# Performance work log

Measured on AMD Instinct MI355X. Metric: run time of the kernel, lower is better.

The kernel has to match this reference:

```python
import jax, jax.numpy as jnp
import numpy as np

EMB = 1024
HID = 2048
N_EXPERTS = 8
CAPACITY_FACTOR = 1.25
Z_LOSS_COEFF = 0.001


def setup_inputs() -> dict:
    key = jax.random.key(0)
    ks = jax.random.split(key, 8)
    B, T = 8, 4096
    x = jax.random.normal(ks[0], (B, T, EMB), dtype=jnp.float32)
    s_r = 1.0 / np.sqrt(EMB)
    s_h = 1.0 / np.sqrt(HID)
    wr = jax.random.uniform(ks[1], (EMB, N_EXPERTS), jnp.float32, -s_r, s_r)
    br = jax.random.uniform(ks[2], (N_EXPERTS,), jnp.float32, -s_r, s_r)
    w1 = jax.random.uniform(ks[3], (N_EXPERTS, EMB, HID), jnp.float32, -s_r, s_r)
    b1 = jax.random.uniform(ks[4], (N_EXPERTS, HID), jnp.float32, -s_r, s_r)
    w2 = jax.random.uniform(ks[5], (N_EXPERTS, HID, EMB), jnp.float32, -s_h, s_h)
    b2 = jax.random.uniform(ks[6], (N_EXPERTS, EMB), jnp.float32, -s_h, s_h)
    return {"x": x, "wr": wr, "br": br, "w1": w1, "b1": b1, "w2": w2, "b2": b2, "k": 2}


def reference(x, wr, br, w1, b1, w2, b2, k):
    B, T, D = x.shape
    E = wr.shape[1]
    N = B * T
    cap = int(CAPACITY_FACTOR * N / E)

    # Router
    logits = jnp.einsum("btd,de->bte", x, wr) + br
    probs = jax.nn.softmax(logits, axis=-1)
    z_loss = Z_LOSS_COEFF * jnp.mean(logits * logits)
    _, topk_idx = jax.lax.top_k(probs, k)  # [B,T,k]

    xf = x.reshape(N, D)
    idx = topk_idx.reshape(N, k)

    # mask[e, n]: token n routed to expert e (any of its top-k slots)
    mask = (idx[None, :, :] == jnp.arange(E, dtype=idx.dtype)[:, None, None]).any(-1)
    pos = jnp.cumsum(mask.astype(jnp.int32), axis=1) - 1  # rank within expert (flattened order)
    keep = mask & (pos < cap)  # capacity truncation: keep first `cap` tokens per expert

    # buf[e, c] = flat index of c-th kept token for expert e, or N (pad)
    cols = jnp.where(keep, pos, cap)  # dropped/unrouted tokens go to dump column
    rows = jnp.broadcast_to(jnp.arange(E)[:, None], (E, N))
    toks_id = jnp.broadcast_to(jnp.arange(N, dtype=jnp.int32)[None, :], (E, N))
    buf = jnp.full((E, cap + 1), N, dtype=jnp.int32).at[rows, cols].set(toks_id)[:, :cap]

    # Dispatch (gather), per-expert dense FFN, combine (scatter-add)
    x_pad = jnp.concatenate([xf, jnp.zeros((1, D), x.dtype)], axis=0)
    toks = x_pad[buf]  # [E, cap, D]
    h = jax.nn.gelu(jnp.einsum("ecd,edh->ech", toks, w1) + b1[:, None, :], approximate=False)
    out = jnp.einsum("ech,ehd->ecd", h, w2) + b2[:, None, :]  # [E, cap, D]
    out_flat = jnp.zeros((N + 1, D), x.dtype).at[buf.reshape(-1)].add(out.reshape(-1, D))[:N]
    output = out_flat.reshape(B, T, D)

    expert_usage = keep.sum(axis=1).astype(jnp.float32)  # [E]
    load = expert_usage / (expert_usage.sum() + 1e-6)
    balance_loss = E * jnp.sum(load * load)
    return output, balance_loss + z_loss, expert_usage
```

## Files before the change

kernel.cpp:

```cpp
#include <hip/hip_runtime.h>
#include <cstdint>

#define NTOK   32768
#define EMB_D  1024
#define HID_H  2048
#define NEXP   8
#define CAP    5120
#define MROWS  (NEXP * CAP)
#define NCHUNK 32

typedef __bf16 bf16_t;
typedef bf16_t bf16x8 __attribute__((ext_vector_type(8)));
typedef float  f32x4  __attribute__((ext_vector_type(4)));

typedef __attribute__((address_space(3))) void       lds_void_t;
typedef const __attribute__((address_space(1))) void g_void_t;

__device__ __forceinline__ void gload_lds16(const void* g, void* l) {
    __builtin_amdgcn_global_load_lds((g_void_t*)(uintptr_t)g,
                                     (lds_void_t*)(uint32_t)(uintptr_t)l, 16, 0, 0);
}

__global__ void router_kernel(const float* __restrict__ x, const float* __restrict__ wr,
                              const float* __restrict__ br, int2* __restrict__ top2,
                              float* __restrict__ zsum) {
    __shared__ float s_wr[NEXP * EMB_D];
    __shared__ float s_z[4];
    const int tid = threadIdx.x;
    for (int i = tid; i < NEXP * EMB_D; i += 256) {
        int d = i >> 3, e = i & 7;
        s_wr[e * EMB_D + d] = wr[i];
    }
    __syncthreads();
    const int wid = tid >> 6, lane = tid & 63;
    const int t = blockIdx.x * 4 + wid;
    const float* xr = x + (size_t)t * EMB_D;

    float acc[NEXP];
#pragma unroll
    for (int e = 0; e < NEXP; e++) acc[e] = 0.f;
#pragma unroll
    for (int it = 0; it < EMB_D / 64; ++it) {
        float xv = xr[lane + 64 * it];
#pragma unroll
        for (int e = 0; e < NEXP; e++) acc[e] += xv * s_wr[e * EMB_D + lane + 64 * it];
    }
#pragma unroll
    for (int e = 0; e < NEXP; e++) {
        float v = acc[e];
#pragma unroll
        for (int off = 32; off > 0; off >>= 1) v += __shfl_xor(v, off);
        acc[e] = v;
    }
    if (lane == 0) {
        float lg[NEXP]; float zs = 0.f;
#pragma unroll
        for (int e = 0; e < NEXP; e++) { lg[e] = acc[e] + br[e]; zs += lg[e] * lg[e]; }
        s_z[wid] = zs;
        float mx = lg[0];
        for (int e = 1; e < NEXP; e++) mx = fmaxf(mx, lg[e]);
        float p[NEXP]; float se = 0.f;
        for (int e = 0; e < NEXP; e++) { p[e] = expf(lg[e] - mx); se += p[e]; }
        for (int e = 0; e < NEXP; e++) p[e] = p[e] / se;
        int i0 = 0; float b0 = p[0];
        for (int e = 1; e < NEXP; e++) if (p[e] > b0) { b0 = p[e]; i0 = e; }
        int i1 = -1; float b1v = -1.f;
        for (int e = 0; e < NEXP; e++) if (e != i0 && p[e] > b1v) { b1v = p[e]; i1 = e; }
        top2[t] = make_int2(i0, i1);
    }
    __syncthreads();
    if (tid == 0) unsafeAtomicAdd(zsum, s_z[0] + s_z[1] + s_z[2] + s_z[3]);
}

__global__ void count_kernel(const int2* __restrict__ top2, int* __restrict__ counts) {
    const int chunk = blockIdx.x;
    const int tid = threadIdx.x;
    const int wid = tid >> 6, lane = tid & 63;
    __shared__ int wcnt[NEXP][16];
    const int2 tp = top2[chunk * 1024 + tid];
#pragma unroll
    for (int e = 0; e < NEXP; e++) {
        const bool m = (tp.x == e) || (tp.y == e);
        unsigned long long bal = __ballot(m);
        if (lane == 0) wcnt[e][wid] = __popcll(bal);
    }
    __syncthreads();
    if (tid < NEXP) {
        int s = 0;
        for (int w = 0; w < 16; w++) s += wcnt[tid][w];
        counts[chunk * NEXP + tid] = s;
    }
}

__global__ void prefix_kernel(const int* __restrict__ counts, int* __restrict__ base,
                              int* __restrict__ usage) {
    const int e = threadIdx.x;
    if (e < NEXP) {
        int run = 0;
        for (int c = 0; c < NCHUNK; c++) {
            base[c * NEXP + e] = run;
            run += counts[c * NEXP + e];
        }
        usage[e] = run < CAP ? run : CAP;
    }
}

__global__ void place_kernel(const int2* __restrict__ top2, const int* __restrict__ base,
                             int* __restrict__ buf, int* __restrict__ inv) {
    const int chunk = blockIdx.x;
    const int tid = threadIdx.x;
    const int wid = tid >> 6, lane = tid & 63;
    const int t = chunk * 1024 + tid;
    __shared__ int wpre[NEXP][16];
    const int2 tp = top2[t];
    int lpre[NEXP]; bool mm[NEXP];
#pragma unroll
    for (int e = 0; e < NEXP; e++) {
        mm[e] = (tp.x == e) || (tp.y == e);
        unsigned long long bal = __ballot(mm[e]);
        lpre[e] = __popcll(bal & ((1ull << lane) - 1ull));
        if (lane == 0) wpre[e][wid] = __popcll(bal);
    }
    __syncthreads();
    if (tid < NEXP) {
        int a = 0;
        for (int w = 0; w < 16; w++) { int v = wpre[tid][w]; wpre[tid][w] = a; a += v; }
    }
    __syncthreads();
#pragma unroll
    for (int e = 0; e < NEXP; e++) {
        if (mm[e]) {
            const int pos = base[chunk * NEXP + e] + wpre[e][wid] + lpre[e];
            const int slot = (tp.x == e) ? 0 : 1;
            if (pos < CAP) {
                const int row = e * CAP + pos;
                buf[row] = t;
                inv[t * 2 + slot] = row;
            } else {
                inv[t * 2 + slot] = -1;
            }
        }
    }
}

__global__ void pad_kernel(const int* __restrict__ usage, int* __restrict__ buf) {
    const int e = blockIdx.x;
    const int u = usage[e];
    for (int p = u + threadIdx.x; p < CAP; p += blockDim.x) buf[e * CAP + p] = NTOK;
}

__global__ void gather_kernel(const float* __restrict__ x, const int* __restrict__ buf,
                              bf16_t* __restrict__ Xg) {
    const int row = blockIdx.x;
    const int t = buf[row];
    const int tid = threadIdx.x;
    bf16x8 v;
    if (t >= 0 && t < NTOK) {
        const float* xr = x + (size_t)t * EMB_D + tid * 8;
        const float4 a = *(const float4*)(xr);
        const float4 b = *(const float4*)(xr + 4);
        v[0] = (bf16_t)a.x; v[1] = (bf16_t)a.y; v[2] = (bf16_t)a.z; v[3] = (bf16_t)a.w;
        v[4] = (bf16_t)b.x; v[5] = (bf16_t)b.y; v[6] = (bf16_t)b.z; v[7] = (bf16_t)b.w;
    } else {
#pragma unroll
        for (int i = 0; i < 8; i++) v[i] = (bf16_t)0.f;
    }
    *(bf16x8*)(Xg + (size_t)row * EMB_D + tid * 8) = v;
}

__global__ void transpose_conv_kernel(const float* __restrict__ in, bf16_t* __restrict__ out,
                                      int R, int C) {
    __shared__ bf16_t tile[64][72];
    const int e = blockIdx.z;
    const int c0 = blockIdx.x * 64, r0 = blockIdx.y * 64;
    const float*  ip = in  + (size_t)e * R * C;
    bf16_t*       op = out + (size_t)e * R * C;
    const int tid = threadIdx.x;
    const int tr = tid >> 4;
    const int tc = (tid & 15) * 4;
#pragma unroll
    for (int rr = 0; rr < 64; rr += 16) {
        const float4 v = *(const float4*)(ip + (size_t)(r0 + tr + rr) * C + (c0 + tc));
        tile[tr + rr][tc + 0] = (bf16_t)v.x;
        tile[tr + rr][tc + 1] = (bf16_t)v.y;
        tile[tr + rr][tc + 2] = (bf16_t)v.z;
        tile[tr + rr][tc + 3] = (bf16_t)v.w;
    }
    __syncthreads();
    const int oc = tid >> 2;
    const int og = (tid & 3) * 16;
    bf16x8 v0, v1;
#pragma unroll
    for (int i = 0; i < 8; i++) v0[i] = tile[og + i][oc];
#pragma unroll
    for (int i = 0; i < 8; i++) v1[i] = tile[og + 8 + i][oc];
    *(bf16x8*)(op + (size_t)(c0 + oc) * R + r0 + og)     = v0;
    *(bf16x8*)(op + (size_t)(c0 + oc) * R + r0 + og + 8) = v1;
}

#define BUF_BYTES 65536
#define LDS_TOTAL 131072

__device__ __forceinline__ const bf16x8* fragp(const char* base, int row, int ks, int quad) {
    return (const bf16x8*)(base + row * 128 + ((((ks << 2) + quad) ^ (row & 7)) << 4));
}

__device__ __forceinline__ void stage_ht(const bf16_t* __restrict__ Ap,
                                         const bf16_t* __restrict__ Bp,
                                         int K, int NT, char* lds0, int idx, int tid) {
    if (idx >= 4 * NT) return;
    const int t = idx >> 2, part = idx & 3;
    char* dst = lds0 + (t & 1) * BUF_BYTES + ((part < 2) ? 32768 : 0)
              + (part & 1) * 16384 + tid * 16;
    const int row0 = tid >> 3;
    const int sq   = (tid & 7) ^ (row0 & 7);
    const bf16_t* src = ((part < 2) ? Bp : Ap)
                      + (size_t)((part & 1) * 128 + row0) * K + (size_t)t * 64 + sq * 8;
    gload_lds16(src, dst);
    gload_lds16(src + (size_t)64 * K, dst + 8192);
}

template <int NT>
__device__ __forceinline__ void mainloop256(const bf16_t* __restrict__ Ap,
                                            const bf16_t* __restrict__ Bp,
                                            char* lds0, f32x4 (&acc)[8][4]) {
    const int K = NT * 64;
    const int tid = threadIdx.x;
    const int lane = tid & 63, wid = tid >> 6;
    const int wm = wid >> 2, wn = wid & 3;
    const int quad = lane >> 4, l16 = lane & 15;

#pragma unroll
    for (int idx = 0; idx < 6; ++idx) stage_ht(Ap, Bp, K, NT, lds0, idx, tid);
    asm volatile("s_waitcnt vmcnt(4)" ::: "memory");
    __builtin_amdgcn_s_barrier();

    bf16x8 a[8], bl[4], bh[4];
    for (int t = 0; t < NT; ++t) {
        const char* bufA = lds0 + (t & 1) * BUF_BYTES;
        const char* bufB = bufA + 32768;
        const int pbase = 4 * t + 6;

#pragma unroll
        for (int mf = 0; mf < 4; ++mf)
#pragma unroll
            for (int ks = 0; ks < 2; ++ks)
                a[mf * 2 + ks] = *fragp(bufA, wm * 128 + mf * 16 + l16, ks, quad);
#pragma unroll
        for (int nf = 0; nf < 2; ++nf)
#pragma unroll
            for (int ks = 0; ks < 2; ++ks)
                bl[nf * 2 + ks] = *fragp(bufB, wn * 64 + nf * 16 + l16, ks, quad);
        stage_ht(Ap, Bp, K, NT, lds0, pbase + 0, tid);
        __builtin_amdgcn_s_barrier();
        asm volatile("s_waitcnt lgkmcnt(0)" ::: "memory");
        __builtin_amdgcn_sched_barrier(0);
        __builtin_amdgcn_s_setprio(1);
#pragma unroll
        for (int mf = 0; mf < 4; ++mf)
#pragma unroll
            for (int nf = 0; nf < 2; ++nf)
#pragma unroll
                for (int ks = 0; ks < 2; ++ks)
                    acc[mf][nf] = __builtin_amdgcn_mfma_f32_16x16x32_bf16(
                        a[mf * 2 + ks], bl[nf * 2 + ks], acc[mf][nf], 0, 0, 0);
        __builtin_amdgcn_s_setprio(0);
        __builtin_amdgcn_s_barrier();

#pragma unroll
        for (int nf = 0; nf < 2; ++nf)
#pragma unroll
            for (int ks = 0; ks < 2; ++ks)
                bh[nf * 2 + ks] = *fragp(bufB, wn * 64 + (nf + 2) * 16 + l16, ks, quad);
        stage_ht(Ap, Bp, K, NT, lds0, pbase + 1, tid);
        __builtin_amdgcn_s_barrier();
        asm volatile("s_waitcnt lgkmcnt(0)" ::: "memory");
        __builtin_amdgcn_sched_barrier(0);
        __builtin_amdgcn_s_setprio(1);
#pragma unroll
        for (int mf = 0; mf < 4; ++mf)
#pragma unroll
            for (int nf = 0; nf < 2; ++nf)
#pragma unroll
                for (int ks = 0; ks < 2; ++ks)
                    acc[mf][nf + 2] = __builtin_amdgcn_mfma_f32_16x16x32_bf16(
                        a[mf * 2 + ks], bh[nf * 2 + ks], acc[mf][nf + 2], 0, 0, 0);
        __builtin_amdgcn_s_setprio(0);
        __builtin_amdgcn_s_barrier();

#pragma unroll
        for (int mf = 0; mf < 4; ++mf)
#pragma unroll
            for (int ks = 0; ks < 2; ++ks)
                a[mf * 2 + ks] = *fragp(bufA, wm * 128 + (mf + 4) * 16 + l16, ks, quad);
        stage_ht(Ap, Bp, K, NT, lds0, pbase + 2, tid);
        __builtin_amdgcn_s_barrier();
        asm volatile("s_waitcnt lgkmcnt(0)" ::: "memory");
        __builtin_amdgcn_sched_barrier(0);
        __builtin_amdgcn_s_setprio(1);
#pragma unroll
        for (int mf = 0; mf < 4; ++mf)
#pragma unroll
            for (int nf = 0; nf < 2; ++nf)
#pragma unroll
                for (int ks = 0; ks < 2; ++ks)
                    acc[mf + 4][nf + 2] = __builtin_amdgcn_mfma_f32_16x16x32_bf16(
                        a[mf * 2 + ks], bh[nf * 2 + ks], acc[mf + 4][nf + 2], 0, 0, 0);
        __builtin_amdgcn_s_setprio(0);
        __builtin_amdgcn_s_barrier();

        stage_ht(Ap, Bp, K, NT, lds0, pbase + 3, tid);
        __builtin_amdgcn_s_setprio(1);
#pragma unroll
        for (int mf = 0; mf < 4; ++mf)
#pragma unroll
            for (int nf = 0; nf < 2; ++nf)
#pragma unroll
                for (int ks = 0; ks < 2; ++ks)
                    acc[mf + 4][nf] = __builtin_amdgcn_mfma_f32_16x16x32_bf16(
                        a[mf * 2 + ks], bl[nf * 2 + ks], acc[mf + 4][nf], 0, 0, 0);
        __builtin_amdgcn_s_setprio(0);
        asm volatile("s_waitcnt vmcnt(4)" ::: "memory");
        __builtin_amdgcn_s_barrier();
    }
}

__global__ __launch_bounds__(512, 2) void gemm1_kernel(const bf16_t* __restrict__ Xg,
                                                       const bf16_t* __restrict__ w1t,
                                                       const float* __restrict__ b1,
                                                       bf16_t* __restrict__ H) {
    extern __shared__ char lds0[];
    const int bn = blockIdx.x, bm = blockIdx.y;
    const int e = bm / (CAP / 256);
    const bf16_t* Ap = Xg + (size_t)bm * 256 * EMB_D;
    const bf16_t* Bp = w1t + ((size_t)e * HID_H + bn * 256) * EMB_D;
    f32x4 acc[8][4];
    const f32x4 z4 = {0.f, 0.f, 0.f, 0.f};
#pragma unroll
    for (int i = 0; i < 8; i++)
#pragma unroll
        for (int j = 0; j < 4; j++) acc[i][j] = z4;

    mainloop256<EMB_D / 64>(Ap, Bp, lds0, acc);

    const int tid = threadIdx.x;
    const int lane = tid & 63, wid = tid >> 6;
    const int wm = wid >> 2, wn = wid & 3;
    const int quad = lane >> 4, l16 = lane & 15;
#pragma unroll
    for (int nf = 0; nf < 4; ++nf) {
        const int col = bn * 256 + wn * 64 + nf * 16 + l16;
        const float bias = b1[e * HID_H + col];
#pragma unroll
        for (int mf = 0; mf < 8; ++mf) {
            const int row = bm * 256 + wm * 128 + mf * 16 + quad * 4;
#pragma unroll
            for (int r = 0; r < 4; ++r) {
                const float v = acc[mf][nf][r] + bias;
                const float g = 0.5f * v * (1.f + erff(v * 0.7071067811865475f));
                H[(size_t)(row + r) * HID_H + col] = (bf16_t)g;
            }
        }
    }
}

__global__ __launch_bounds__(512, 2) void gemm2_kernel(const bf16_t* __restrict__ H,
                                                       const bf16_t* __restrict__ w2t,
                                                       bf16_t* __restrict__ Yg) {
    extern __shared__ char lds0[];
    const int bn = blockIdx.x, bm = blockIdx.y;
    const int e = bm / (CAP / 256);
    const bf16_t* Ap = H + (size_t)bm * 256 * HID_H;
    const bf16_t* Bp = w2t + ((size_t)e * EMB_D + bn * 256) * HID_H;
    f32x4 acc[8][4];
    const f32x4 z4 = {0.f, 0.f, 0.f, 0.f};
#pragma unroll
    for (int i = 0; i < 8; i++)
#pragma unroll
        for (int j = 0; j < 4; j++) acc[i][j] = z4;

    mainloop256<HID_H / 64>(Ap, Bp, lds0, acc);

    const int tid = threadIdx.x;
    const int lane = tid & 63, wid = tid >> 6;
    const int wm = wid >> 2, wn = wid & 3;
    const int quad = lane >> 4, l16 = lane & 15;
#pragma unroll
    for (int nf = 0; nf < 4; ++nf) {
        const int col = bn * 256 + wn * 64 + nf * 16 + l16;
#pragma unroll
        for (int mf = 0; mf < 8; ++mf) {
            const int row = bm * 256 + wm * 128 + mf * 16 + quad * 4;
#pragma unroll
            for (int r = 0; r < 4; ++r)
                Yg[(size_t)(row + r) * EMB_D + col] = (bf16_t)acc[mf][nf][r];
        }
    }
}

__global__ void combine_kernel(const bf16_t* __restrict__ Yg, const float* __restrict__ b2,
                               const int* __restrict__ inv, float* __restrict__ out) {
    const int t = blockIdx.x;
    const int tid = threadIdx.x;
    const int d = tid * 8;
    const int r0 = inv[t * 2], r1 = inv[t * 2 + 1];
    float acc[8];
#pragma unroll
    for (int i = 0; i < 8; i++) acc[i] = 0.f;
    if (r0 >= 0) {
        const int e = r0 / CAP;
        const bf16x8 v = *(const bf16x8*)(Yg + (size_t)r0 * EMB_D + d);
        const float* bp = b2 + e * EMB_D + d;
#pragma unroll
        for (int i = 0; i < 8; i++) acc[i] += (float)v[i] + bp[i];
    }
    if (r1 >= 0) {
        const int e = r1 / CAP;
        const bf16x8 v = *(const bf16x8*)(Yg + (size_t)r1 * EMB_D + d);
        const float* bp = b2 + e * EMB_D + d;
#pragma unroll
        for (int i = 0; i < 8; i++) acc[i] += (float)v[i] + bp[i];
    }
    float4 o0 = {acc[0], acc[1], acc[2], acc[3]};
    float4 o1 = {acc[4], acc[5], acc[6], acc[7]};
    *(float4*)(out + (size_t)t * EMB_D + d)     = o0;
    *(float4*)(out + (size_t)t * EMB_D + d + 4) = o1;
}

__global__ void finalize_kernel(const int* __restrict__ usage, const float* __restrict__ zsum,
                                float* __restrict__ out) {
    if (threadIdx.x == 0) {
        float u[NEXP], s = 0.f;
        for (int e = 0; e < NEXP; e++) { u[e] = (float)usage[e]; s += u[e]; }
        const float inv = 1.f / (s + 1e-6f);
        float bal = 0.f;
        for (int e = 0; e < NEXP; e++) { const float l = u[e] * inv; bal += l * l; }
        bal *= (float)NEXP;
        const float z = 0.001f * zsum[0] / (float)((size_t)NTOK * NEXP);
        out[(size_t)NTOK * EMB_D] = bal + z;
        for (int e = 0; e < NEXP; e++) out[(size_t)NTOK * EMB_D + 1 + e] = u[e];
    }
}

extern "C" void kernel_launch(void* const* d_in, const int* in_sizes, int n_in,
                              void* d_out, int out_size, void* d_ws, size_t ws_size,
                              hipStream_t stream) {
    (void)in_sizes; (void)n_in; (void)out_size;
    const float* x  = (const float*)d_in[0];
    const float* wr = (const float*)d_in[1];
    const float* br = (const float*)d_in[2];
    const float* w1 = (const float*)d_in[3];
    const float* b1 = (const float*)d_in[4];
    const float* w2 = (const float*)d_in[5];
    const float* b2 = (const float*)d_in[6];
    float* out = (float*)d_out;

    uint8_t* ws = (uint8_t*)d_ws;
    size_t off = 0;
    auto carve = [&](size_t bytes) -> void* {
        off = (off + 255) & ~(size_t)255;
        void* p = ws + off;
        off += bytes;
        return p;
    };
    float*  zsum  = (float*)carve(sizeof(float));
    int*    usage = (int*)carve(NEXP * sizeof(int));
    int*    counts = (int*)carve((size_t)NCHUNK * NEXP * sizeof(int));
    int*    base   = (int*)carve((size_t)NCHUNK * NEXP * sizeof(int));
    int2*   top2 = (int2*)carve((size_t)NTOK * sizeof(int2));
    int*    buf  = (int*)carve((size_t)MROWS * sizeof(int));
    int*    inv  = (int*)carve((size_t)NTOK * 2 * sizeof(int));
    bf16_t* Xg   = (bf16_t*)carve((size_t)MROWS * EMB_D * sizeof(bf16_t));
    bf16_t* w1t  = (bf16_t*)carve((size_t)NEXP * HID_H * EMB_D * sizeof(bf16_t));
    bf16_t* w2t  = (bf16_t*)carve((size_t)NEXP * EMB_D * HID_H * sizeof(bf16_t));
    bf16_t* H    = (bf16_t*)carve((size_t)MROWS * HID_H * sizeof(bf16_t));
    bf16_t* Yg   = Xg;
    if (off > ws_size) return;

    static bool attr_set = false;
    if (!attr_set) {
        hipFuncSetAttribute(reinterpret_cast<const void*>(&gemm1_kernel),
                            hipFuncAttributeMaxDynamicSharedMemorySize, LDS_TOTAL);
        hipFuncSetAttribute(reinterpret_cast<const void*>(&gemm2_kernel),
                            hipFuncAttributeMaxDynamicSharedMemorySize, LDS_TOTAL);
        attr_set = true;
    }

    hipMemsetAsync(zsum, 0, sizeof(float), stream);

    router_kernel<<<NTOK / 4, 256, 0, stream>>>(x, wr, br, top2, zsum);
    count_kernel<<<NCHUNK, 1024, 0, stream>>>(top2, counts);
    prefix_kernel<<<1, 64, 0, stream>>>(counts, base, usage);
    place_kernel<<<NCHUNK, 1024, 0, stream>>>(top2, base, buf, inv);
    pad_kernel<<<NEXP, 256, 0, stream>>>(usage, buf);
    gather_kernel<<<MROWS, 128, 0, stream>>>(x, buf, Xg);
    transpose_conv_kernel<<<dim3(HID_H / 64, EMB_D / 64, NEXP), 256, 0, stream>>>(w1, w1t, EMB_D, HID_H);
    transpose_conv_kernel<<<dim3(EMB_D / 64, HID_H / 64, NEXP), 256, 0, stream>>>(w2, w2t, HID_H, EMB_D);
    gemm1_kernel<<<dim3(HID_H / 256, MROWS / 256), 512, LDS_TOTAL, stream>>>(Xg, w1t, b1, H);
    gemm2_kernel<<<dim3(EMB_D / 256, MROWS / 256), 512, LDS_TOTAL, stream>>>(H, w2t, Yg);
    combine_kernel<<<NTOK, 128, 0, stream>>>(Yg, b2, inv, out);
    finalize_kernel<<<1, 64, 0, stream>>>(usage, zsum, out);
}
```

Measured before the change: 907.6 us.

## Restructure GEMM mainloop into two half-phases and stage epilogue through LDS

```diff
diff --git a/kernel.cpp b/kernel.cpp
--- a/kernel.cpp
+++ b/kernel.cpp
@@ -205,19 +205,17 @@
     return (const bf16x8*)(base + row * 128 + ((((ks << 2) + quad) ^ (row & 7)) << 4));
 }
 
-__device__ __forceinline__ void stage_ht(const bf16_t* __restrict__ Ap,
-                                         const bf16_t* __restrict__ Bp,
-                                         int K, int NT, char* lds0, int idx, int tid) {
-    if (idx >= 4 * NT) return;
-    const int t = idx >> 2, part = idx & 3;
-    char* dst = lds0 + (t & 1) * BUF_BYTES + ((part < 2) ? 32768 : 0)
-              + (part & 1) * 16384 + tid * 16;
+__device__ __forceinline__ void stage_panel(const bf16_t* __restrict__ P, int K,
+                                            char* lds0, int dstpar, int isB,
+                                            int srct, int tid) {
+    char* dst = lds0 + dstpar * BUF_BYTES + (isB ? 32768 : 0) + tid * 16;
     const int row0 = tid >> 3;
     const int sq   = (tid & 7) ^ (row0 & 7);
-    const bf16_t* src = ((part < 2) ? Bp : Ap)
-                      + (size_t)((part & 1) * 128 + row0) * K + (size_t)t * 64 + sq * 8;
+    const bf16_t* src = P + (size_t)row0 * K + (size_t)srct * 64 + sq * 8;
     gload_lds16(src, dst);
-    gload_lds16(src + (size_t)64 * K, dst + 8192);
+    gload_lds16(src + (size_t)64 * K,  dst + 8192);
+    gload_lds16(src + (size_t)128 * K, dst + 16384);
+    gload_lds16(src + (size_t)192 * K, dst + 24576);
 }
 
 template <int NT>
@@ -230,98 +228,112 @@
     const int wm = wid >> 2, wn = wid & 3;
     const int quad = lane >> 4, l16 = lane & 15;
 
-#pragma unroll
-    for (int idx = 0; idx < 6; ++idx) stage_ht(Ap, Bp, K, NT, lds0, idx, tid);
+    stage_panel(Bp, K, lds0, 0, 1, 0, tid);
+    stage_panel(Ap, K, lds0, 0, 0, 0, tid);
+    stage_panel(Bp, K, lds0, 1, 1, (NT > 1 ? 1 : 0), tid);
     asm volatile("s_waitcnt vmcnt(4)" ::: "memory");
     __builtin_amdgcn_s_barrier();
 
-    bf16x8 a[8], bl[4], bh[4];
+    bf16x8 aa[8], bb[8];
     for (int t = 0; t < NT; ++t) {
         const char* bufA = lds0 + (t & 1) * BUF_BYTES;
         const char* bufB = bufA + 32768;
-        const int pbase = 4 * t + 6;
 
 #pragma unroll
         for (int mf = 0; mf < 4; ++mf)
 #pragma unroll
             for (int ks = 0; ks < 2; ++ks)
-                a[mf * 2 + ks] = *fragp(bufA, wm * 128 + mf * 16 + l16, ks, quad);
-#pragma unroll
-        for (int nf = 0; nf < 2; ++nf)
+                aa[mf * 2 + ks] = *fragp(bufA, wm * 128 + mf * 16 + l16, ks, quad);
+#pragma unroll
+        for (int nf = 0; nf < 4; ++nf)
 #pragma unroll
             for (int ks = 0; ks < 2; ++ks)
-                bl[nf * 2 + ks] = *fragp(bufB, wn * 64 + nf * 16 + l16, ks, quad);
-        stage_ht(Ap, Bp, K, NT, lds0, pbase + 0, tid);
-        __builtin_amdgcn_s_barrier();
+                bb[nf * 2 + ks] = *fragp(bufB, wn * 64 + nf * 16 + l16, ks, quad);
+        stage_panel(Ap, K, lds0, (t + 1) & 1, 0, (t + 1 < NT ? t + 1 : 0), tid);
         asm volatile("s_waitcnt lgkmcnt(0)" ::: "memory");
         __builtin_amdgcn_sched_barrier(0);
         __builtin_amdgcn_s_setprio(1);
 #pragma unroll
         for (int mf = 0; mf < 4; ++mf)
 #pragma unroll
-            for (int nf = 0; nf < 2; ++nf)
+            for (int nf = 0; nf < 4; ++nf)
 #pragma unroll
                 for (int ks = 0; ks < 2; ++ks)
                     acc[mf][nf] = __builtin_amdgcn_mfma_f32_16x16x32_bf16(
-                        a[mf * 2 + ks], bl[nf * 2 + ks], acc[mf][nf], 0, 0, 0);
+                        aa[mf * 2 + ks], bb[nf * 2 + ks], acc[mf][nf], 0, 0, 0);
         __builtin_amdgcn_s_setprio(0);
         __builtin_amdgcn_s_barrier();
 
 #pragma unroll
-        for (int nf = 0; nf < 2; ++nf)
+        for (int mf = 0; mf < 4; ++mf)
 #pragma unroll
             for (int ks = 0; ks < 2; ++ks)
-                bh[nf * 2 + ks] = *fragp(bufB, wn * 64 + (nf + 2) * 16 + l16, ks, quad);
-        stage_ht(Ap, Bp, K, NT, lds0, pbase + 1, tid);
-        __builtin_amdgcn_s_barrier();
+                aa[mf * 2 + ks] = *fragp(bufA, wm * 128 + (mf + 4) * 16 + l16, ks, quad);
+        stage_panel(Bp, K, lds0, t & 1, 1, (t + 2 < NT ? t + 2 : t + 2 - NT), tid);
         asm volatile("s_waitcnt lgkmcnt(0)" ::: "memory");
         __builtin_amdgcn_sched_barrier(0);
         __builtin_amdgcn_s_setprio(1);
 #pragma unroll
         for (int mf = 0; mf < 4; ++mf)
 #pragma unroll
-            for (int nf = 0; nf < 2; ++nf)
-#pragma unroll
-                for (int ks = 0; ks < 2; ++ks)
-                    acc[mf][nf + 2] = __builtin_amdgcn_mfma_f32_16x16x32_bf16(
-                        a[mf * 2 + ks], bh[nf * 2 + ks], acc[mf][nf + 2], 0, 0, 0);
-        __builtin_amdgcn_s_setprio(0);
-        __builtin_amdgcn_s_barrier();
-
-#pragma unroll
-        for (int mf = 0; mf < 4; ++mf)
-#pragma unroll
-            for (int ks = 0; ks < 2; ++ks)
-                a[mf * 2 + ks] = *fragp(bufA, wm * 128 + (mf + 4) * 16 + l16, ks, quad);
-        stage_ht(Ap, Bp, K, NT, lds0, pbase + 2, tid);
-        __builtin_amdgcn_s_barrier();
-        asm volatile("s_waitcnt lgkmcnt(0)" ::: "memory");
-        __builtin_amdgcn_sched_barrier(0);
-        __builtin_amdgcn_s_setprio(1);
-#pragma unroll
-        for (int mf = 0; mf < 4; ++mf)
-#pragma unroll
-            for (int nf = 0; nf < 2; ++nf)
-#pragma unroll
-                for (int ks = 0; ks < 2; ++ks)
-                    acc[mf + 4][nf + 2] = __builtin_amdgcn_mfma_f32_16x16x32_bf16(
-                        a[mf * 2 + ks], bh[nf * 2 + ks], acc[mf + 4][nf + 2], 0, 0, 0);
-        __builtin_amdgcn_s_setprio(0);
-        __builtin_amdgcn_s_barrier();
-
-        stage_ht(Ap, Bp, K, NT, lds0, pbase + 3, tid);
-        __builtin_amdgcn_s_setprio(1);
-#pragma unroll
-        for (int mf = 0; mf < 4; ++mf)
-#pragma unroll
-            for (int nf = 0; nf < 2; ++nf)
+            for (int nf = 0; nf < 4; ++nf)
 #pragma unroll
                 for (int ks = 0; ks < 2; ++ks)
                     acc[mf + 4][nf] = __builtin_amdgcn_mfma_f32_16x16x32_bf16(
-                        a[mf * 2 + ks], bl[nf * 2 + ks], acc[mf + 4][nf], 0, 0, 0);
+                        aa[mf * 2 + ks], bb[nf * 2 + ks], acc[mf + 4][nf], 0, 0, 0);
         __builtin_amdgcn_s_setprio(0);
         asm volatile("s_waitcnt vmcnt(4)" ::: "memory");
         __builtin_amdgcn_s_barrier();
+    }
+    asm volatile("s_waitcnt vmcnt(0)" ::: "memory");
+    __builtin_amdgcn_s_barrier();
+}
+
+template <int APPLY>
+__device__ __forceinline__ void epilogue_store(const f32x4 (&acc)[8][4], char* lds0,
+                                               const float* __restrict__ bias4,
+                                               bf16_t* __restrict__ Out, int ldo,
+                                               int bm, int bn) {
+    const int tid = threadIdx.x;
+    const int lane = tid & 63, wid = tid >> 6;
+    const int wm = wid >> 2, wn = wid & 3;
+    const int quad = lane >> 4, l16 = lane & 15;
+    const int l8 = lane & 7, g8 = lane >> 3;
+    char* eb = lds0 + wid * 8192;
+    const int rslot = (l8 ^ g8) << 4;
+#pragma unroll
+    for (int h = 0; h < 2; ++h) {
+#pragma unroll
+        for (int mfh = 0; mfh < 4; ++mfh) {
+#pragma unroll
+            for (int r = 0; r < 4; ++r) {
+                const int lrow = mfh * 16 + quad * 4 + r;
+#pragma unroll
+                for (int nf = 0; nf < 4; ++nf) {
+                    float v = acc[h * 4 + mfh][nf][r];
+                    if (APPLY) {
+                        v += bias4[nf];
+                        v = 0.5f * v * (1.f + erff(v * 0.7071067811865475f));
+                    }
+                    const int lcol = nf * 16 + l16;
+                    const int byte = lrow * 128 +
+                        (((lcol >> 3) ^ (lrow & 7)) << 4) + ((lcol & 7) << 1);
+                    *(bf16_t*)(eb + byte) = (bf16_t)v;
+                }
+            }
+        }
+        asm volatile("s_waitcnt lgkmcnt(0)" ::: "memory");
+        __builtin_amdgcn_sched_barrier(0);
+#pragma unroll
+        for (int i = 0; i < 8; ++i) {
+            const int rr = i * 8 + g8;
+            const bf16x8 v = *(const bf16x8*)(eb + rr * 128 + rslot);
+            const int grow = bm * 256 + wm * 128 + h * 64 + rr;
+            const int gcol = bn * 256 + wn * 64 + l8 * 8;
+            *(bf16x8*)(Out + (size_t)grow * ldo + gcol) = v;
+        }
+        asm volatile("s_waitcnt lgkmcnt(0)" ::: "memory");
+        __builtin_amdgcn_sched_barrier(0);
     }
 }
 
@@ -343,25 +355,13 @@
 
     mainloop256<EMB_D / 64>(Ap, Bp, lds0, acc);
 
-    const int tid = threadIdx.x;
-    const int lane = tid & 63, wid = tid >> 6;
-    const int wm = wid >> 2, wn = wid & 3;
-    const int quad = lane >> 4, l16 = lane & 15;
-#pragma unroll
-    for (int nf = 0; nf < 4; ++nf) {
-        const int col = bn * 256 + wn * 64 + nf * 16 + l16;
-        const float bias = b1[e * HID_H + col];
-#pragma unroll
-        for (int mf = 0; mf < 8; ++mf) {
-            const int row = bm * 256 + wm * 128 + mf * 16 + quad * 4;
-#pragma unroll
-            for (int r = 0; r < 4; ++r) {
-                const float v = acc[mf][nf][r] + bias;
-                const float g = 0.5f * v * (1.f + erff(v * 0.7071067811865475f));
-                H[(size_t)(row + r) * HID_H + col] = (bf16_t)g;
-            }
-        }
-    }
+    const int lane = threadIdx.x & 63, wid = threadIdx.x >> 6;
+    const int wn = wid & 3, l16 = lane & 15;
+    float bias4[4];
+#pragma unroll
+    for (int nf = 0; nf < 4; ++nf)
+        bias4[nf] = b1[e * HID_H + bn * 256 + wn * 64 + nf * 16 + l16];
+    epilogue_store<1>(acc, lds0, bias4, H, HID_H, bm, bn);
 }
 
 __global__ __launch_bounds__(512, 2) void gemm2_kernel(const bf16_t* __restrict__ H,
@@ -381,21 +381,7 @@
 
     mainloop256<HID_H / 64>(Ap, Bp, lds0, acc);
 
-    const int tid = threadIdx.x;
-    const int lane = tid & 63, wid = tid >> 6;
-    const int wm = wid >> 2, wn = wid & 3;
-    const int quad = lane >> 4, l16 = lane & 15;
-#pragma unroll
-    for (int nf = 0; nf < 4; ++nf) {
-        const int col = bn * 256 + wn * 64 + nf * 16 + l16;
-#pragma unroll
-        for (int mf = 0; mf < 8; ++mf) {
-            const int row = bm * 256 + wm * 128 + mf * 16 + quad * 4;
-#pragma unroll
-            for (int r = 0; r < 4; ++r)
-                Yg[(size_t)(row + r) * EMB_D + col] = (bf16_t)acc[mf][nf][r];
-        }
-    }
+    epilogue_store<0>(acc, lds0, nullptr, Yg, EMB_D, bm, bn);
 }
 
 __global__ void combine_kernel(const bf16_t* __restrict__ Yg, const float* __restrict__ b2,
```

Result: faster. 861.9 us (-5.0%).
